# Optimization experiments

Hardware: AMD Instinct MI355X
Metric: run time of the kernel (lower is better)

The kernel has to match this reference:

```python
import jax, jax.numpy as jnp
import numpy as np

USER_NUM = 100000
ITEM_NUM = 150000
N_NODES = USER_NUM + ITEM_NUM
EMB = 64
N_LAYERS = 3
N_EDGES = 1200000


def setup_inputs() -> dict:
    key = jax.random.key(0)
    k1, k2, k3, k4, k5 = jax.random.split(key, 5)
    user_emb = jax.random.normal(k1, (USER_NUM, EMB), dtype=jnp.float32) * 0.1
    item_emb = jax.random.normal(k2, (ITEM_NUM, EMB), dtype=jnp.float32) * 0.1
    adj_rows = jax.random.randint(k3, (N_EDGES,), 0, N_NODES, dtype=jnp.int32)
    adj_cols = jax.random.randint(k4, (N_EDGES,), 0, N_NODES, dtype=jnp.int32)
    # normalized-adjacency-like positive values
    adj_vals = jax.random.uniform(k5, (N_EDGES,), dtype=jnp.float32) * 0.1
    return {"user_emb": user_emb, "item_emb": item_emb,
            "adj_rows": adj_rows, "adj_cols": adj_cols, "adj_vals": adj_vals}


def _spmm(rows, cols, vals, embeds):
    # out[r] += vals[e] * embeds[cols[e]]  — torch.spmm(adj, embeds) with COO adj
    msgs = vals[:, None] * embeds[cols]           # [E, d]
    return jax.ops.segment_sum(msgs, rows, num_segments=N_NODES)


def reference(user_emb, item_emb, adj_rows, adj_cols, adj_vals):
    # forward_graphcl: concat embeddings, n_layers spmm hops, sum all hop outputs
    embeds = jnp.concatenate([user_emb, item_emb], axis=0)  # [N, d]
    main = embeds
    cur = embeds
    for _ in range(N_LAYERS):
        cur = _spmm(adj_rows, adj_cols, adj_vals, cur)
        main = main + cur
    return main
```

## Files before the change

kernel.cpp:

```cpp
#include <hip/hip_runtime.h>
#include <hip/hip_fp16.h>

#define USER_NUM 100000
#define ITEM_NUM 150000
#define N_NODES  250000
#define EMB      64
#define N_EDGES  1200000
#define N_ELEM   (N_NODES * EMB)

#define NBLK1 512
#define NBUCK 245
#define CAP   8192
#define TB1   4096
#define INIT_TILES 3907
#define SST   2048

typedef float f4 __attribute__((ext_vector_type(4)));
typedef int   i4 __attribute__((ext_vector_type(4)));

__global__ __launch_bounds__(256) void bin_init_kernel(
    const int* __restrict__ rows, const int* __restrict__ cols,
    const float* __restrict__ vals,
    int* __restrict__ chunkcur, int* __restrict__ bucket_cnt,
    int2* __restrict__ tmp,
    const float* __restrict__ user, const float* __restrict__ item,
    __half* __restrict__ emb16)
{
    __shared__ int  scnt[256];
    __shared__ int  spref[256];
    __shared__ int  schunk[NBUCK];
    __shared__ unsigned char sbuck[TB1];
    __shared__ int2 tilebuf[TB1];

    int t = threadIdx.x;

    if (blockIdx.x >= NBLK1) {
        int gi = (blockIdx.x - NBLK1) * 256 + t;
        if (gi < N_ELEM / 16) {
            int base = gi * 16;
            const int UE = USER_NUM * EMB;
            const f4* src = (base < UE) ? (const f4*)(user + base)
                                        : (const f4*)(item + (base - UE));
            f4 f0 = __builtin_nontemporal_load(src);
            f4 f1 = __builtin_nontemporal_load(src + 1);
            f4 f2 = __builtin_nontemporal_load(src + 2);
            f4 f3 = __builtin_nontemporal_load(src + 3);
            union { i4 v; __half2 h[4]; } a, b;
            a.h[0] = __float22half2_rn(make_float2(f0.x, f0.y));
            a.h[1] = __float22half2_rn(make_float2(f0.z, f0.w));
            a.h[2] = __float22half2_rn(make_float2(f1.x, f1.y));
            a.h[3] = __float22half2_rn(make_float2(f1.z, f1.w));
            b.h[0] = __float22half2_rn(make_float2(f2.x, f2.y));
            b.h[1] = __float22half2_rn(make_float2(f2.z, f2.w));
            b.h[2] = __float22half2_rn(make_float2(f3.x, f3.y));
            b.h[3] = __float22half2_rn(make_float2(f3.z, f3.w));
            ((i4*)(emb16 + base))[0] = a.v;
            ((i4*)(emb16 + base))[1] = b.v;
        }
        return;
    }

    int b = blockIdx.x;
    int e0 = (int)((long long)b * N_EDGES / NBLK1);
    int e1 = (int)((long long)(b + 1) * N_EDGES / NBLK1);

    scnt[t] = 0;
    __syncthreads();
    for (int e = e0 + t; e < e1; e += 256)
        atomicAdd(&scnt[rows[e] >> 10], 1);
    __syncthreads();
    int realc = (t < NBUCK) ? scnt[t] : 0;
    int v     = (realc + 7) & ~7;
    __syncthreads();
    spref[t] = v;
    __syncthreads();
    for (int off = 1; off < 256; off <<= 1) {
        int u = (t >= off) ? spref[t - off] : 0;
        __syncthreads();
        spref[t] += u;
        __syncthreads();
    }
    int excl = spref[t] - v;
    __syncthreads();
    spref[t] = excl;
    __syncthreads();
    int padded_total = spref[NBUCK];

    scnt[t] = excl;
    if (t < NBUCK) {
        schunk[t] = (v > 0) ? atomicAdd(&chunkcur[t], v >> 3) : 0;
        if (realc > 0) atomicAdd(&bucket_cnt[t], realc);
        for (int k = realc; k < v; ++k) tilebuf[excl + k] = make_int2(-1, 0);
        for (int k = 0; k < v; ++k)     sbuck[excl + k] = (unsigned char)t;
    }
    __syncthreads();
    for (int e = e0 + t; e < e1; e += 256) {
        int r  = rows[e];
        int lp = atomicAdd(&scnt[r >> 10], 1);
        tilebuf[lp] = make_int2(((r & 1023) << 18) | cols[e], __float_as_int(vals[e]));
    }
    __syncthreads();
    for (int j = t; j < padded_total; j += 256) {
        int lo = sbuck[j];
        tmp[(size_t)lo * CAP + schunk[lo] * 8 + (j - spref[lo])] = tilebuf[j];
    }
}

__global__ __launch_bounds__(256) void place4_kernel(
    const int* __restrict__ chunkcur, const int* __restrict__ bucket_cnt,
    const int2* __restrict__ tmp,
    int* __restrict__ row_ptr, int2* __restrict__ edges)
{
    __shared__ int  shist[1024];
    __shared__ int  swave[256];
    __shared__ int2 sstage[SST];

    int t = threadIdx.x;
    int b = blockIdx.x >> 2;
    int s = blockIdx.x & 3;

    int vv = (t < NBUCK) ? bucket_cnt[t] : 0;
    swave[t] = vv;
    __syncthreads();
    for (int off = 1; off < 256; off <<= 1) {
        int u = (t >= off) ? swave[t - off] : 0;
        __syncthreads();
        swave[t] += u;
        __syncthreads();
    }
    int bb  = (b == 0) ? 0 : swave[b - 1];
    int cnt = swave[b] - bb;
    __syncthreads();

    for (int i = t; i < 1024; i += 256) shist[i] = 0;
    __syncthreads();

    int nrec = chunkcur[b] * 8;
    const int2* src = tmp + (size_t)b * CAP;
    for (int j = t; j < nrec; j += 256) {
        int x = src[j].x;
        if (x != -1) atomicAdd(&shist[x >> 18], 1);
    }
    __syncthreads();

    int h0 = shist[4 * t], h1 = shist[4 * t + 1];
    int h2 = shist[4 * t + 2], h3 = shist[4 * t + 3];
    int sum = h0 + h1 + h2 + h3;
    swave[t] = sum;
    __syncthreads();
    for (int off = 1; off < 256; off <<= 1) {
        int u = (t >= off) ? swave[t - off] : 0;
        __syncthreads();
        swave[t] += u;
        __syncthreads();
    }
    int base = bb + swave[t] - sum;
    __syncthreads();
    shist[4 * t]     = base;
    shist[4 * t + 1] = base + h0;
    shist[4 * t + 2] = base + h0 + h1;
    shist[4 * t + 3] = base + h0 + h1 + h2;
    __syncthreads();

    int wstart = shist[s * 256];
    int wend   = (s < 3) ? shist[(s + 1) * 256] : bb + cnt;
    {
        int idx = b * 1024 + s * 256 + t;
        if (idx < N_NODES) row_ptr[idx] = shist[s * 256 + t];
    }
    if (blockIdx.x == 0 && t == 0) row_ptr[N_NODES] = N_EDGES;
    __syncthreads();

    for (int j = t; j < nrec; j += 256) {
        int2 rec = src[j];
        int  rl  = rec.x >> 18;
        if (rec.x != -1 && (rl >> 8) == s) {
            int lp = atomicAdd(&shist[rl], 1) - wstart;
            sstage[lp] = make_int2(rec.x & 0x3FFFF, rec.y);
        }
    }
    __syncthreads();
    for (int j = t; j < wend - wstart; j += 256)
        edges[wstart + j] = sstage[j];
}

template <int MODE>
__global__ __launch_bounds__(256) void spmm_kernel(
    const int* __restrict__ row_ptr, const int2* __restrict__ edges,
    const __half* __restrict__ in16, const __half* __restrict__ emb16,
    const __half* __restrict__ cur1,
    float* __restrict__ out, __half* __restrict__ cur_out)
{
    int t = blockIdx.x * blockDim.x + threadIdx.x;
    int r = t >> 4;
    int l = t & 15;
    if (r >= N_NODES) return;
    int start = row_ptr[r];
    int end   = row_ptr[r + 1];
    int idx   = r * EMB + 4 * l;

    union { int2 i; __half2 h[2]; } pe, p1, p2;
    if (MODE == 1) {
        pe.i = *(const int2*)(emb16 + idx);
        p1.i = *(const int2*)(cur1 + idx);
        p2.i = *(const int2*)(in16 + idx);
    }

    float ax = 0.f, ay = 0.f, az = 0.f, aw = 0.f;
    for (int j = start; j < end; j += 8) {
        int2 e[8];
#pragma unroll
        for (int k = 0; k < 8; ++k) e[k] = edges[j + k];
#pragma unroll
        for (int k = 0; k < 8; ++k) {
            bool ok = (j + k < end);
            int   c = ok ? e[k].x : 0;
            float v = ok ? __int_as_float(e[k].y) : 0.0f;
            union { int2 i; __half2 h[2]; } g;
            g.i = *(const int2*)(in16 + c * EMB + 4 * l);
            float2 x0 = __half22float2(g.h[0]);
            float2 x1 = __half22float2(g.h[1]);
            ax += v * x0.x; ay += v * x0.y;
            az += v * x1.x; aw += v * x1.y;
        }
    }

    if (MODE == 0) {
        union { int2 i; __half2 h[2]; } o;
        o.h[0] = __float22half2_rn(make_float2(ax, ay));
        o.h[1] = __float22half2_rn(make_float2(az, aw));
        *(int2*)(cur_out + idx) = o.i;
    } else {
        float2 e0 = __half22float2(pe.h[0]), e1 = __half22float2(pe.h[1]);
        float2 c0 = __half22float2(p1.h[0]), c1 = __half22float2(p1.h[1]);
        float2 d0 = __half22float2(p2.h[0]), d1 = __half22float2(p2.h[1]);
        float4 o = make_float4(e0.x + c0.x + d0.x + ax,
                               e0.y + c0.y + d0.y + ay,
                               e1.x + c1.x + d1.x + az,
                               e1.y + c1.y + d1.y + aw);
        *(float4*)(out + idx) = o;
    }
}

extern "C" void kernel_launch(void* const* d_in, const int* in_sizes, int n_in,
                              void* d_out, int out_size, void* d_ws, size_t ws_size,
                              hipStream_t stream) {
    const float* user = (const float*)d_in[0];
    const float* item = (const float*)d_in[1];
    const int*   rows = (const int*)d_in[2];
    const int*   cols = (const int*)d_in[3];
    const float* vals = (const float*)d_in[4];
    float*       out  = (float*)d_out;

    char* p = (char*)d_ws;
    __half* emb16   = (__half*)p;  p += (size_t)N_ELEM * 2;
    __half* cur1    = (__half*)p;  p += (size_t)N_ELEM * 2;
    __half* cur2    = (__half*)p;  p += (size_t)N_ELEM * 2;
    int2*   tmp     = (int2*)p;    p += (size_t)NBUCK * CAP * 8;
    int2*   edges   = (int2*)p;    p += (size_t)(N_EDGES + 32) * 8;
    int*    row_ptr = (int*)p;     p += 1000448;
    int*    bucket_cnt = (int*)p;  p += 1024;
    int*    chunkcur   = (int*)p;  p += 1024;

    hipMemsetAsync(bucket_cnt, 0, 2048, stream);

    bin_init_kernel<<<NBLK1 + INIT_TILES, 256, 0, stream>>>(
        rows, cols, vals, chunkcur, bucket_cnt, tmp, user, item, emb16);
    place4_kernel<<<NBUCK * 4, 256, 0, stream>>>(
        chunkcur, bucket_cnt, tmp, row_ptr, edges);

    const int spmm_blocks = (N_NODES * 16 + 255) / 256;
    spmm_kernel<0><<<spmm_blocks, 256, 0, stream>>>(row_ptr, edges, emb16, emb16, cur1, out, cur1);
    spmm_kernel<0><<<spmm_blocks, 256, 0, stream>>>(row_ptr, edges, cur1, emb16, cur1, out, cur2);
    spmm_kernel<1><<<spmm_blocks, 256, 0, stream>>>(row_ptr, edges, cur2, emb16, cur1, out, nullptr);
}
```

Baseline: 286.7 us.

## Fuse first SpMM hop into CSR placement kernel using staged shared-memory edges

The first SpMM layer is now computed inside the placement kernel, reading the per-row edge records straight from the shared-memory staging buffer instead of re-reading them from global memory in a separate launch. This removes one kernel launch and one global pass over the edge list. In exchange, each placement block does more serial work, since 16 groups of 16 lanes loop over 256 rows. Occupancy is limited by the large shared staging buffer, which could lengthen the placement phase.

```diff
diff --git a/kernel.cpp b/kernel.cpp
--- a/kernel.cpp
+++ b/kernel.cpp
@@ -106,10 +106,11 @@
     }
 }
 
-__global__ __launch_bounds__(256) void place4_kernel(
+__global__ __launch_bounds__(256) void place_spmm1_kernel(
     const int* __restrict__ chunkcur, const int* __restrict__ bucket_cnt,
     const int2* __restrict__ tmp,
-    int* __restrict__ row_ptr, int2* __restrict__ edges)
+    int* __restrict__ row_ptr, int2* __restrict__ edges,
+    const __half* __restrict__ emb16, __half* __restrict__ cur1)
 {
     __shared__ int  shist[1024];
     __shared__ int  swave[256];
@@ -164,6 +165,7 @@
 
     int wstart = shist[s * 256];
     int wend   = (s < 3) ? shist[(s + 1) * 256] : bb + cnt;
+    swave[t] = shist[s * 256 + t];
     {
         int idx = b * 1024 + s * 256 + t;
         if (idx < N_NODES) row_ptr[idx] = shist[s * 256 + t];
@@ -182,6 +184,31 @@
     __syncthreads();
     for (int j = t; j < wend - wstart; j += 256)
         edges[wstart + j] = sstage[j];
+    __syncthreads();
+
+    int qw = t >> 4;
+    int l  = t & 15;
+    for (int i = qw; i < 256; i += 16) {
+        int r = b * 1024 + s * 256 + i;
+        if (r >= N_NODES) continue;
+        int st = swave[i] - wstart;
+        int en = shist[s * 256 + i] - wstart;
+        float ax = 0.f, ay = 0.f, az = 0.f, aw = 0.f;
+        for (int j = st; j < en; ++j) {
+            int2 rec = sstage[j];
+            float v  = __int_as_float(rec.y);
+            union { int2 i; __half2 h[2]; } g;
+            g.i = *(const int2*)(emb16 + rec.x * EMB + 4 * l);
+            float2 x0 = __half22float2(g.h[0]);
+            float2 x1 = __half22float2(g.h[1]);
+            ax += v * x0.x; ay += v * x0.y;
+            az += v * x1.x; aw += v * x1.y;
+        }
+        union { int2 i; __half2 h[2]; } o;
+        o.h[0] = __float22half2_rn(make_float2(ax, ay));
+        o.h[1] = __float22half2_rn(make_float2(az, aw));
+        *(int2*)(cur1 + r * EMB + 4 * l) = o.i;
+    }
 }
 
 template <int MODE>
@@ -266,11 +293,10 @@
 
     bin_init_kernel<<<NBLK1 + INIT_TILES, 256, 0, stream>>>(
         rows, cols, vals, chunkcur, bucket_cnt, tmp, user, item, emb16);
-    place4_kernel<<<NBUCK * 4, 256, 0, stream>>>(
-        chunkcur, bucket_cnt, tmp, row_ptr, edges);
+    place_spmm1_kernel<<<NBUCK * 4, 256, 0, stream>>>(
+        chunkcur, bucket_cnt, tmp, row_ptr, edges, emb16, cur1);
 
     const int spmm_blocks = (N_NODES * 16 + 255) / 256;
-    spmm_kernel<0><<<spmm_blocks, 256, 0, stream>>>(row_ptr, edges, emb16, emb16, cur1, out, cur1);
     spmm_kernel<0><<<spmm_blocks, 256, 0, stream>>>(row_ptr, edges, cur1, emb16, cur1, out, cur2);
     spmm_kernel<1><<<spmm_blocks, 256, 0, stream>>>(row_ptr, edges, cur2, emb16, cur1, out, nullptr);
 }
```

Result: slower. 303.4 us (+5.8%).
